# Kernel tuning notes

Measured on AMD Instinct MI355X. Metric: run time of the kernel, lower is better.

## Reference

```python
import jax, jax.numpy as jnp
import numpy as np

NUM_ITERATIONS = 3

def _squash(s):
    # Original squash reduces over the trailing singleton dim -> elementwise.
    sn = s * s
    return sn * s / ((1.0 + sn) * jnp.sqrt(sn))

def setup_inputs() -> dict:
    key = jax.random.key(0)
    k1, k2 = jax.random.split(key)
    x = jax.random.normal(k1, (128, 1152, 8), dtype=jnp.float32)
    W = jax.random.normal(k2, (1, 1152, 16, 16, 8), dtype=jnp.float32)
    return {"x": x, "W": W}

def reference(x, W):
    # x: [B, R, I]; W: [1, R, C, O, I]
    Wr = W[0]  # [R, C, O, I]
    # u_hat = W @ x broadcast over capsules: [B, R, C, O]
    u_hat = jnp.einsum('rcoi,bri->brco', Wr, x)
    R, C = Wr.shape[0], Wr.shape[1]
    b = jnp.zeros((R, C), dtype=x.dtype)  # routing logits (shared across batch)
    v = None
    for it in range(NUM_ITERATIONS):
        # legacy F.softmax on [1,R,C,1] -> dim=1 == routes axis
        c = jax.nn.softmax(b, axis=0)  # [R, C]
        s = jnp.einsum('rc,brco->bco', c, u_hat)  # [B, C, O]
        v = _squash(s)
        if it < NUM_ITERATIONS - 1:
            # agreement: <u_hat, v> averaged over batch
            a = jnp.einsum('brco,bco->brc', u_hat, v).mean(axis=0)  # [R, C]
            b = b + a
    return v  # [B, C, O] == v_j.squeeze(1).squeeze(-1)
```

## Files before the change

kernel.cpp:

```cpp
#include <hip/hip_runtime.h>
#include <math.h>

#define B_   128
#define R_   1152
#define C_   16
#define O_   16
#define RS_  96
#define RCH_ 12
#define NBLK 768
#define SLICE_P 8464

#define WS_SP   0
#define WS_V    3250176
#define WS_BLOG 3282944
#define WS_CTRL 3301376
#define WS_WT   3302144

__device__ __forceinline__ float squashf(float s) {
    return s * fabsf(s) / (1.0f + s * s);
}

__global__ __launch_bounds__(512) void wtrans_k(const float* __restrict__ W,
                                                float* __restrict__ wt,
                                                float* __restrict__ ctrl) {
    const int r = blockIdx.x;
    const int t = threadIdx.x;
    __shared__ float4 sh[520];
    const float4* __restrict__ W4 = (const float4*)W;
    float4* __restrict__ Wt4 = (float4*)wt;

    if (r == 0) {
        for (int u = t; u < 768; u += 512) ctrl[u] = 0.0f;
    }

    sh[(t & 7) * 65 + (t >> 3)] = W4[r * 512 + t];
    __syncthreads();
    Wt4[r * 512 + t] = sh[(t >> 6) * 65 + (t & 63)];
}

template <bool FIRST>
__global__ __launch_bounds__(256) void gemm_s_k(const float* __restrict__ x,
                                                const float* __restrict__ wt,
                                                const float* __restrict__ blog,
                                                const float* __restrict__ colsum,
                                                float* __restrict__ sp) {
    const int bid = blockIdx.x;
    const int xcd = bid & 7;
    const int g   = bid >> 3;
    const int rs  = xcd * 12 + g % 12;
    const int bt  = g / 12;
    const int t   = threadIdx.x;
    const int co4 = t & 63;
    const int b4  = t >> 6;
    const int c   = co4 >> 2;
    const int r0  = rs * RCH_;

    __shared__ float4 xl4[16 * RCH_ * 2];
    __shared__ float  cwl[RCH_ * 16];
    __shared__ float  colinv_sh[16];

    const float4* __restrict__ X4  = (const float4*)x;
    const float4* __restrict__ Wt4 = (const float4*)wt;

    #pragma unroll
    for (int k = 0; k < 2; ++k) {
        const int u = t + k * 256;
        if (u < 16 * RCH_ * 2) {
            const int bl = u / (RCH_ * 2), rem = u % (RCH_ * 2);
            xl4[u] = X4[((bt * 16 + bl) * R_ + r0) * 2 + rem];
        }
    }

    if (!FIRST) {
        if (t < 16) colinv_sh[t] = 1.0f / colsum[t * 16];
        __syncthreads();
        if (t < RCH_ * 16) {
            const int rl = t >> 4, cc = t & 15;
            cwl[t] = __expf(blog[(r0 + rl) * 16 + cc]) * colinv_sh[cc];
        }
    }
    __syncthreads();

    float acc[4][4];
    #pragma unroll
    for (int j = 0; j < 4; ++j)
        #pragma unroll
        for (int q = 0; q < 4; ++q) acc[j][q] = 0.f;

    const float4* __restrict__ wbase = Wt4 + ((size_t)r0 << 9) + co4;

    auto body = [&](int rr, const float4* wv) {
        const float cwv = FIRST ? (1.0f / (float)R_) : cwl[rr * 16 + c];
        #pragma unroll
        for (int j = 0; j < 4; ++j) {
            const float4 xa = xl4[(b4 * 4 + j) * (RCH_ * 2) + rr * 2];
            const float4 xb = xl4[(b4 * 4 + j) * (RCH_ * 2) + rr * 2 + 1];
            const float d0 = wv[0].x*xa.x + wv[0].y*xa.y + wv[0].z*xa.z + wv[0].w*xa.w
                           + wv[1].x*xb.x + wv[1].y*xb.y + wv[1].z*xb.z + wv[1].w*xb.w;
            const float d1 = wv[2].x*xa.x + wv[2].y*xa.y + wv[2].z*xa.z + wv[2].w*xa.w
                           + wv[3].x*xb.x + wv[3].y*xb.y + wv[3].z*xb.z + wv[3].w*xb.w;
            const float d2 = wv[4].x*xa.x + wv[4].y*xa.y + wv[4].z*xa.z + wv[4].w*xa.w
                           + wv[5].x*xb.x + wv[5].y*xb.y + wv[5].z*xb.z + wv[5].w*xb.w;
            const float d3 = wv[6].x*xa.x + wv[6].y*xa.y + wv[6].z*xa.z + wv[6].w*xa.w
                           + wv[7].x*xb.x + wv[7].y*xb.y + wv[7].z*xb.z + wv[7].w*xb.w;
            acc[j][0] = fmaf(cwv, d0, acc[j][0]);
            acc[j][1] = fmaf(cwv, d1, acc[j][1]);
            acc[j][2] = fmaf(cwv, d2, acc[j][2]);
            acc[j][3] = fmaf(cwv, d3, acc[j][3]);
        }
    };

    float4 w[8];
    #pragma unroll
    for (int q = 0; q < 8; ++q) w[q] = wbase[q * 64];
    for (int rr = 0; rr < RCH_ - 1; ++rr) {
        float4 wn[8];
        const float4* wp = wbase + ((size_t)(rr + 1) << 9);
        #pragma unroll
        for (int q = 0; q < 8; ++q) wn[q] = wp[q * 64];
        body(rr, w);
        #pragma unroll
        for (int q = 0; q < 8; ++q) w[q] = wn[q];
    }
    body(RCH_ - 1, w);

    float4* sp4 = (float4*)sp;
    #pragma unroll
    for (int j = 0; j < 4; ++j) {
        const int b = bt * 16 + b4 * 4 + j;
        float4 o4; o4.x = acc[j][0]; o4.y = acc[j][1]; o4.z = acc[j][2]; o4.w = acc[j][3];
        sp4[(size_t)rs * SLICE_P + b * 64 + co4] = o4;
    }
}

__global__ __launch_bounds__(256) void reduce_squash_k(const float* __restrict__ sp,
                                                       float* __restrict__ dst) {
    const int out4 = blockIdx.x * 256 + threadIdx.x;
    const float4* __restrict__ sp4 = (const float4*)sp;
    float ax = 0.f, ay = 0.f, az = 0.f, aw = 0.f;
    #pragma unroll 16
    for (int k = 0; k < RS_; ++k) {
        const float4 u = sp4[(size_t)k * SLICE_P + out4];
        ax += u.x; ay += u.y; az += u.z; aw += u.w;
    }
    float4 o;
    o.x = squashf(ax); o.y = squashf(ay); o.z = squashf(az); o.w = squashf(aw);
    ((float4*)dst)[out4] = o;
}

template <bool FIRST>
__global__ __launch_bounds__(256, 4) void a_k(const float* __restrict__ x,
                                              const float* __restrict__ wt,
                                              const float* __restrict__ v,
                                              float* __restrict__ blog,
                                              float* __restrict__ colsum) {
    const int r = blockIdx.x;
    const int t = threadIdx.x;
    const int w = t >> 6, lane = t & 63;
    const int co4 = lane, c = lane >> 2;

    __shared__ float4 xl[256];
    __shared__ float  red[64];
    const float4* __restrict__ X4  = (const float4*)x;
    const float4* __restrict__ V4  = (const float4*)v;
    const float4* __restrict__ Wt4 = (const float4*)wt;

    {
        const int b = t >> 1, rem = t & 1;
        xl[t] = X4[(b * R_ + r) * 2 + rem];
    }
    __syncthreads();

    float y[8][4];
    #pragma unroll
    for (int i = 0; i < 8; ++i)
        #pragma unroll
        for (int q = 0; q < 4; ++q) y[i][q] = 0.f;

    const int b0 = w * 32;
    #pragma unroll 4
    for (int bb = 0; bb < 32; ++bb) {
        const int b = b0 + bb;
        const float4 xa = xl[b * 2];
        const float4 xb = xl[b * 2 + 1];
        const float4 vv = V4[b * 64 + co4];
        const float xs[8] = {xa.x, xa.y, xa.z, xa.w, xb.x, xb.y, xb.z, xb.w};
        #pragma unroll
        for (int i = 0; i < 8; ++i) {
            y[i][0] = fmaf(xs[i], vv.x, y[i][0]);
            y[i][1] = fmaf(xs[i], vv.y, y[i][1]);
            y[i][2] = fmaf(xs[i], vv.z, y[i][2]);
            y[i][3] = fmaf(xs[i], vv.w, y[i][3]);
        }
    }

    const float4* wp = Wt4 + ((size_t)r << 9) + co4;
    float part = 0.f;
    #pragma unroll
    for (int q = 0; q < 4; ++q) {
        const float4 w0 = wp[(2 * q) * 64];
        const float4 w1 = wp[(2 * q + 1) * 64];
        part += w0.x*y[0][q] + w0.y*y[1][q] + w0.z*y[2][q] + w0.w*y[3][q]
              + w1.x*y[4][q] + w1.y*y[5][q] + w1.z*y[6][q] + w1.w*y[7][q];
    }
    part += __shfl_xor(part, 1);
    part += __shfl_xor(part, 2);
    if ((lane & 3) == 0) red[w * 16 + c] = part;
    __syncthreads();
    if (t < 16) {
        const float val = ((red[t] + red[16 + t]) + (red[32 + t] + red[48 + t]))
                          * (1.0f / (float)B_);
        const int idx = r * 16 + t;
        const float nv = FIRST ? val : (blog[idx] + val);
        blog[idx] = nv;
        atomicAdd(&colsum[t * 16], __expf(nv));
    }
}

extern "C" void kernel_launch(void* const* d_in, const int* in_sizes, int n_in,
                              void* d_out, int out_size, void* d_ws, size_t ws_size,
                              hipStream_t stream) {
    const float* x = (const float*)d_in[0];
    const float* W = (const float*)d_in[1];
    float* out = (float*)d_out;
    float* ws  = (float*)d_ws;

    float* sp   = ws + WS_SP;
    float* v    = ws + WS_V;
    float* blog = ws + WS_BLOG;
    float* ctrl = ws + WS_CTRL;
    float* wt   = ws + WS_WT;

    float* cs0 = ctrl + 256;
    float* cs1 = ctrl + 512;

    wtrans_k<<<R_, 512, 0, stream>>>(W, wt, ctrl);

    gemm_s_k<true ><<<NBLK, 256, 0, stream>>>(x, wt, nullptr, nullptr, sp);
    reduce_squash_k<<<32, 256, 0, stream>>>(sp, v);
    a_k<true ><<<R_, 256, 0, stream>>>(x, wt, v, blog, cs0);

    gemm_s_k<false><<<NBLK, 256, 0, stream>>>(x, wt, blog, cs0, sp);
    reduce_squash_k<<<32, 256, 0, stream>>>(sp, v);
    a_k<false><<<R_, 256, 0, stream>>>(x, wt, v, blog, cs1);

    gemm_s_k<false><<<NBLK, 256, 0, stream>>>(x, wt, blog, cs1, sp);
    reduce_squash_k<<<32, 256, 0, stream>>>(sp, out);
}
```

Before: 206.4 us.

## Fuse W transpose into first gemm, widen reduce and a_k, retile partials

```diff
diff --git a/kernel.cpp b/kernel.cpp
--- a/kernel.cpp
+++ b/kernel.cpp
@@ -5,50 +5,34 @@
 #define R_   1152
 #define C_   16
 #define O_   16
-#define RS_  96
-#define RCH_ 12
-#define NBLK 768
+#define RS_  128
+#define RCH_ 9
+#define NBLK 1024
 #define SLICE_P 8464
 
 #define WS_SP   0
-#define WS_V    3250176
-#define WS_BLOG 3282944
-#define WS_CTRL 3301376
-#define WS_WT   3302144
+#define WS_V    4333568
+#define WS_BLOG 4366336
+#define WS_CTRL 4384768
+#define WS_WT   4385536
 
 __device__ __forceinline__ float squashf(float s) {
     return s * fabsf(s) / (1.0f + s * s);
 }
 
-__global__ __launch_bounds__(512) void wtrans_k(const float* __restrict__ W,
-                                                float* __restrict__ wt,
-                                                float* __restrict__ ctrl) {
-    const int r = blockIdx.x;
-    const int t = threadIdx.x;
-    __shared__ float4 sh[520];
-    const float4* __restrict__ W4 = (const float4*)W;
-    float4* __restrict__ Wt4 = (float4*)wt;
-
-    if (r == 0) {
-        for (int u = t; u < 768; u += 512) ctrl[u] = 0.0f;
-    }
-
-    sh[(t & 7) * 65 + (t >> 3)] = W4[r * 512 + t];
-    __syncthreads();
-    Wt4[r * 512 + t] = sh[(t >> 6) * 65 + (t & 63)];
-}
-
-template <bool FIRST>
-__global__ __launch_bounds__(256) void gemm_s_k(const float* __restrict__ x,
-                                                const float* __restrict__ wt,
-                                                const float* __restrict__ blog,
-                                                const float* __restrict__ colsum,
-                                                float* __restrict__ sp) {
+template <int MODE>
+__global__ __launch_bounds__(256, 4) void gemm_s_k(const float* __restrict__ x,
+                                                   const float* __restrict__ W,
+                                                   float* __restrict__ wt,
+                                                   const float* __restrict__ blog,
+                                                   const float* __restrict__ colsum,
+                                                   float* __restrict__ sp,
+                                                   float* __restrict__ ctrl) {
     const int bid = blockIdx.x;
     const int xcd = bid & 7;
     const int g   = bid >> 3;
-    const int rs  = xcd * 12 + g % 12;
-    const int bt  = g / 12;
+    const int rs  = xcd * 16 + (g & 15);
+    const int bt  = g >> 4;
     const int t   = threadIdx.x;
     const int co4 = t & 63;
     const int b4  = t >> 6;
@@ -60,7 +44,12 @@
     __shared__ float  colinv_sh[16];
 
     const float4* __restrict__ X4  = (const float4*)x;
-    const float4* __restrict__ Wt4 = (const float4*)wt;
+    const float4* __restrict__ W4  = (const float4*)W;
+    float4* __restrict__ Wt4 = (float4*)wt;
+
+    if (MODE == 0 && bid == 0) {
+        for (int u = t; u < 768; u += 256) ctrl[u] = 0.0f;
+    }
 
     #pragma unroll
     for (int k = 0; k < 2; ++k) {
@@ -71,7 +60,7 @@
         }
     }
 
-    if (!FIRST) {
+    if (MODE != 0) {
         if (t < 16) colinv_sh[t] = 1.0f / colsum[t * 16];
         __syncthreads();
         if (t < RCH_ * 16) {
@@ -87,42 +76,42 @@
         #pragma unroll
         for (int q = 0; q < 4; ++q) acc[j][q] = 0.f;
 
-    const float4* __restrict__ wbase = Wt4 + ((size_t)r0 << 9) + co4;
-
-    auto body = [&](int rr, const float4* wv) {
-        const float cwv = FIRST ? (1.0f / (float)R_) : cwl[rr * 16 + c];
+    #pragma unroll 3
+    for (int rr = 0; rr < RCH_; ++rr) {
+        float4 w[8];
+        if (MODE == 0) {
+            const float4* wp = W4 + ((size_t)(r0 + rr) << 9) + co4 * 8;
+            #pragma unroll
+            for (int q = 0; q < 8; ++q) w[q] = wp[q];
+            if (bt == 0) {
+                float4* wo = Wt4 + ((size_t)(r0 + rr) << 9) + co4;
+                #pragma unroll
+                for (int q = 0; q < 8; ++q) wo[q * 64] = w[q];
+            }
+        } else {
+            const float4* wp = Wt4 + ((size_t)(r0 + rr) << 9) + co4;
+            #pragma unroll
+            for (int q = 0; q < 8; ++q) w[q] = wp[q * 64];
+        }
+        const float cwv = (MODE == 0) ? (1.0f / (float)R_) : cwl[rr * 16 + c];
         #pragma unroll
         for (int j = 0; j < 4; ++j) {
             const float4 xa = xl4[(b4 * 4 + j) * (RCH_ * 2) + rr * 2];
             const float4 xb = xl4[(b4 * 4 + j) * (RCH_ * 2) + rr * 2 + 1];
-            const float d0 = wv[0].x*xa.x + wv[0].y*xa.y + wv[0].z*xa.z + wv[0].w*xa.w
-                           + wv[1].x*xb.x + wv[1].y*xb.y + wv[1].z*xb.z + wv[1].w*xb.w;
-            const float d1 = wv[2].x*xa.x + wv[2].y*xa.y + wv[2].z*xa.z + wv[2].w*xa.w
-                           + wv[3].x*xb.x + wv[3].y*xb.y + wv[3].z*xb.z + wv[3].w*xb.w;
-            const float d2 = wv[4].x*xa.x + wv[4].y*xa.y + wv[4].z*xa.z + wv[4].w*xa.w
-                           + wv[5].x*xb.x + wv[5].y*xb.y + wv[5].z*xb.z + wv[5].w*xb.w;
-            const float d3 = wv[6].x*xa.x + wv[6].y*xa.y + wv[6].z*xa.z + wv[6].w*xa.w
-                           + wv[7].x*xb.x + wv[7].y*xb.y + wv[7].z*xb.z + wv[7].w*xb.w;
+            const float d0 = w[0].x*xa.x + w[0].y*xa.y + w[0].z*xa.z + w[0].w*xa.w
+                           + w[1].x*xb.x + w[1].y*xb.y + w[1].z*xb.z + w[1].w*xb.w;
+            const float d1 = w[2].x*xa.x + w[2].y*xa.y + w[2].z*xa.z + w[2].w*xa.w
+                           + w[3].x*xb.x + w[3].y*xb.y + w[3].z*xb.z + w[3].w*xb.w;
+            const float d2 = w[4].x*xa.x + w[4].y*xa.y + w[4].z*xa.z + w[4].w*xa.w
+                           + w[5].x*xb.x + w[5].y*xb.y + w[5].z*xb.z + w[5].w*xb.w;
+            const float d3 = w[6].x*xa.x + w[6].y*xa.y + w[6].z*xa.z + w[6].w*xa.w
+                           + w[7].x*xb.x + w[7].y*xb.y + w[7].z*xb.z + w[7].w*xb.w;
             acc[j][0] = fmaf(cwv, d0, acc[j][0]);
             acc[j][1] = fmaf(cwv, d1, acc[j][1]);
             acc[j][2] = fmaf(cwv, d2, acc[j][2]);
             acc[j][3] = fmaf(cwv, d3, acc[j][3]);
         }
-    };
-
-    float4 w[8];
-    #pragma unroll
-    for (int q = 0; q < 8; ++q) w[q] = wbase[q * 64];
-    for (int rr = 0; rr < RCH_ - 1; ++rr) {
-        float4 wn[8];
-        const float4* wp = wbase + ((size_t)(rr + 1) << 9);
-        #pragma unroll
-        for (int q = 0; q < 8; ++q) wn[q] = wp[q * 64];
-        body(rr, w);
-        #pragma unroll
-        for (int q = 0; q < 8; ++q) w[q] = wn[q];
-    }
-    body(RCH_ - 1, w);
+    }
 
     float4* sp4 = (float4*)sp;
     #pragma unroll
@@ -133,19 +122,32 @@
     }
 }
 
-__global__ __launch_bounds__(256) void reduce_squash_k(const float* __restrict__ sp,
-                                                       float* __restrict__ dst) {
-    const int out4 = blockIdx.x * 256 + threadIdx.x;
+__global__ __launch_bounds__(256, 4) void reduce_squash_k(const float* __restrict__ sp,
+                                                          float* __restrict__ dst) {
+    const int t  = threadIdx.x;
+    const int o4 = blockIdx.x * 32 + (t & 31);
+    const int kq = t >> 5;
     const float4* __restrict__ sp4 = (const float4*)sp;
-    float ax = 0.f, ay = 0.f, az = 0.f, aw = 0.f;
-    #pragma unroll 16
-    for (int k = 0; k < RS_; ++k) {
-        const float4 u = sp4[(size_t)k * SLICE_P + out4];
-        ax += u.x; ay += u.y; az += u.z; aw += u.w;
-    }
-    float4 o;
-    o.x = squashf(ax); o.y = squashf(ay); o.z = squashf(az); o.w = squashf(aw);
-    ((float4*)dst)[out4] = o;
+    float4 a; a.x = 0.f; a.y = 0.f; a.z = 0.f; a.w = 0.f;
+    #pragma unroll
+    for (int k = 0; k < 16; ++k) {
+        const float4 u = sp4[(size_t)(kq * 16 + k) * SLICE_P + o4];
+        a.x += u.x; a.y += u.y; a.z += u.z; a.w += u.w;
+    }
+    __shared__ float4 red[256];
+    red[t] = a;
+    __syncthreads();
+    if (t < 32) {
+        float ax = 0.f, ay = 0.f, az = 0.f, aw = 0.f;
+        #pragma unroll
+        for (int j = 0; j < 8; ++j) {
+            const float4 p = red[t + 32 * j];
+            ax += p.x; ay += p.y; az += p.z; aw += p.w;
+        }
+        float4 o;
+        o.x = squashf(ax); o.y = squashf(ay); o.z = squashf(az); o.w = squashf(aw);
+        ((float4*)dst)[o4] = o;
+    }
 }
 
 template <bool FIRST>
@@ -154,20 +156,23 @@
                                               const float* __restrict__ v,
                                               float* __restrict__ blog,
                                               float* __restrict__ colsum) {
-    const int r = blockIdx.x;
-    const int t = threadIdx.x;
-    const int w = t >> 6, lane = t & 63;
+    const int r0 = blockIdx.x * 2;
+    const int t  = threadIdx.x;
+    const int w  = t >> 6, lane = t & 63;
+    const int rr = w & 1, half = w >> 1;
     const int co4 = lane, c = lane >> 2;
 
-    __shared__ float4 xl[256];
+    __shared__ float4 xl[128 * 4];
     __shared__ float  red[64];
     const float4* __restrict__ X4  = (const float4*)x;
     const float4* __restrict__ V4  = (const float4*)v;
     const float4* __restrict__ Wt4 = (const float4*)wt;
 
-    {
-        const int b = t >> 1, rem = t & 1;
-        xl[t] = X4[(b * R_ + r) * 2 + rem];
+    #pragma unroll
+    for (int kk = 0; kk < 2; ++kk) {
+        const int u = t + kk * 256;
+        const int b = u >> 2, rem = u & 3;
+        xl[u] = X4[(b * R_ + r0) * 2 + rem];
     }
     __syncthreads();
 
@@ -177,12 +182,12 @@
         #pragma unroll
         for (int q = 0; q < 4; ++q) y[i][q] = 0.f;
 
-    const int b0 = w * 32;
+    const int b0 = half * 64;
     #pragma unroll 4
-    for (int bb = 0; bb < 32; ++bb) {
+    for (int bb = 0; bb < 64; ++bb) {
         const int b = b0 + bb;
-        const float4 xa = xl[b * 2];
-        const float4 xb = xl[b * 2 + 1];
+        const float4 xa = xl[b * 4 + rr * 2];
+        const float4 xb = xl[b * 4 + rr * 2 + 1];
         const float4 vv = V4[b * 64 + co4];
         const float xs[8] = {xa.x, xa.y, xa.z, xa.w, xb.x, xb.y, xb.z, xb.w};
         #pragma unroll
@@ -194,7 +199,7 @@
         }
     }
 
-    const float4* wp = Wt4 + ((size_t)r << 9) + co4;
+    const float4* wp = Wt4 + ((size_t)(r0 + rr) << 9) + co4;
     float part = 0.f;
     #pragma unroll
     for (int q = 0; q < 4; ++q) {
@@ -207,13 +212,14 @@
     part += __shfl_xor(part, 2);
     if ((lane & 3) == 0) red[w * 16 + c] = part;
     __syncthreads();
-    if (t < 16) {
-        const float val = ((red[t] + red[16 + t]) + (red[32 + t] + red[48 + t]))
+    if (t < 32) {
+        const int rr2 = t >> 4, cc = t & 15;
+        const float val = (red[rr2 * 16 + cc] + red[(2 + rr2) * 16 + cc])
                           * (1.0f / (float)B_);
-        const int idx = r * 16 + t;
+        const int idx = (r0 + rr2) * 16 + cc;
         const float nv = FIRST ? val : (blog[idx] + val);
         blog[idx] = nv;
-        atomicAdd(&colsum[t * 16], __expf(nv));
+        atomicAdd(&colsum[cc * 16], __expf(nv));
     }
 }
 
@@ -234,16 +240,14 @@
     float* cs0 = ctrl + 256;
     float* cs1 = ctrl + 512;
 
-    wtrans_k<<<R_, 512, 0, stream>>>(W, wt, ctrl);
-
-    gemm_s_k<true ><<<NBLK, 256, 0, stream>>>(x, wt, nullptr, nullptr, sp);
-    reduce_squash_k<<<32, 256, 0, stream>>>(sp, v);
-    a_k<true ><<<R_, 256, 0, stream>>>(x, wt, v, blog, cs0);
-
-    gemm_s_k<false><<<NBLK, 256, 0, stream>>>(x, wt, blog, cs0, sp);
-    reduce_squash_k<<<32, 256, 0, stream>>>(sp, v);
-    a_k<false><<<R_, 256, 0, stream>>>(x, wt, v, blog, cs1);
-
-    gemm_s_k<false><<<NBLK, 256, 0, stream>>>(x, wt, blog, cs1, sp);
-    reduce_squash_k<<<32, 256, 0, stream>>>(sp, out);
-}
+    gemm_s_k<0><<<NBLK, 256, 0, stream>>>(x, W, wt, nullptr, nullptr, sp, ctrl);
+    reduce_squash_k<<<256, 256, 0, stream>>>(sp, v);
+    a_k<true ><<<576, 256, 0, stream>>>(x, wt, v, blog, cs0);
+
+    gemm_s_k<1><<<NBLK, 256, 0, stream>>>(x, nullptr, wt, blog, cs0, sp, ctrl);
+    reduce_squash_k<<<256, 256, 0, stream>>>(sp, v);
+    a_k<false><<<576, 256, 0, stream>>>(x, wt, v, blog, cs1);
+
+    gemm_s_k<1><<<NBLK, 256, 0, stream>>>(x, nullptr, wt, blog, cs1, sp, ctrl);
+    reduce_squash_k<<<256, 256, 0, stream>>>(sp, out);
+}
```

Result: slower. 281.9 us (+36.6%).
